# Optimization experiments

Measured on AMD Instinct MI355X. Metric: run time of the kernel, lower is better.

The kernel has to match this reference:

```python
import jax, jax.numpy as jnp
import numpy as np

MARGIN = 1.0


def setup_inputs() -> dict:
    key = jax.random.key(0)
    k1, k2, k3 = jax.random.split(key, 3)
    B, P = 8192, 16
    return {
        "energies": jax.random.normal(k1, (B, 1), dtype=jnp.float32),
        "property_values": jax.random.normal(k2, (B, P), dtype=jnp.float32),
        "property_targets": jax.random.normal(k3, (P,), dtype=jnp.float32),
    }


def reference(energies, property_values, property_targets):
    # distances[i] = ||property_values[i] - property_targets||_2, shape [B]
    distances = jnp.linalg.norm(property_values - property_targets[None, :], axis=-1)
    B = energies.shape[0]
    e = energies[:, 0]  # [B]
    # pair mask: i != j and distances[i] < distances[j]  -> [B, B]
    mask = (distances[:, None] < distances[None, :]) & (~jnp.eye(B, dtype=bool))
    # ranking loss per pair: relu(e_i - e_j + margin)
    pair_loss = jax.nn.relu(e[:, None] - e[None, :] + MARGIN)
    loss_sum = jnp.sum(jnp.where(mask, pair_loss, 0.0))
    count = jnp.sum(mask).astype(jnp.float32)
    loss = loss_sum / jnp.maximum(count, 1.0)
    # torch version accumulates [1]-shaped tensors -> output shape [1]
    return loss[None]
```

## Files before the change

### kernel.cpp

```cpp
#include <hip/hip_runtime.h>
#include <math.h>

#define MARGIN 1.0f
#define NT 256
#define TI 512
#define TJ 256

__global__ __launch_bounds__(NT) void dist_kernel(
    const float* __restrict__ pv,
    const float* __restrict__ pt,
    float* __restrict__ dist,
    float* __restrict__ acc,
    unsigned* __restrict__ counter,
    int B, int P)
{
    if (blockIdx.x == 0 && threadIdx.x == 0) {
        acc[0] = 0.f;
        *counter = 0u;
    }
    int i = blockIdx.x * NT + threadIdx.x;
    if (i >= B) return;
    float s = 0.f;
    if ((P & 3) == 0) {
        const float4* row = (const float4*)(pv + (size_t)i * P);
        const float4* tgt = (const float4*)pt;
        for (int p = 0; p < (P >> 2); ++p) {
            float4 v = row[p];
            float4 t = tgt[p];
            float d0 = v.x - t.x, d1 = v.y - t.y, d2 = v.z - t.z, d3 = v.w - t.w;
            s = fmaf(d0, d0, s); s = fmaf(d1, d1, s);
            s = fmaf(d2, d2, s); s = fmaf(d3, d3, s);
        }
    } else {
        const float* row = pv + (size_t)i * P;
        for (int p = 0; p < P; ++p) {
            float d = row[p] - pt[p];
            s = fmaf(d, d, s);
        }
    }
    dist[i] = sqrtf(s);
}

__global__ __launch_bounds__(NT) void pair_kernel(
    const float* __restrict__ e,
    const float* __restrict__ dist,
    float* __restrict__ acc,
    unsigned* __restrict__ counter,
    float* __restrict__ out,
    int B, int nj)
{
    __shared__ float2 sde[TJ];

    int it = blockIdx.x / nj;
    int jt = blockIdx.x % nj;

    {
        int j = jt * TJ + (int)threadIdx.x;
        bool ok = (j < B);
        float dj = ok ? dist[j] : -INFINITY;
        float ej = ok ? e[j]    : 0.f;
        sde[threadIdx.x] = make_float2(dj, ej);
    }
    __syncthreads();

    int i0 = it * TI + (int)threadIdx.x;
    int i1 = i0 + NT;
    bool ok0 = (i0 < B), ok1 = (i1 < B);
    float d0 = ok0 ? dist[i0] : INFINITY;
    float a0 = ok0 ? (e[i0] + MARGIN) : 0.f;
    float d1 = ok1 ? dist[i1] : INFINITY;
    float a1 = ok1 ? (e[i1] + MARGIN) : 0.f;

    const float4* sde4 = (const float4*)sde;
    float sum = 0.f;
    #pragma unroll 8
    for (int k = 0; k < TJ / 2; ++k) {
        float4 q = sde4[k];
        float w;
        w = (d0 < q.x) ? a0 : -INFINITY;  sum += fmaxf(w - q.y, 0.f);
        w = (d1 < q.x) ? a1 : -INFINITY;  sum += fmaxf(w - q.y, 0.f);
        w = (d0 < q.z) ? a0 : -INFINITY;  sum += fmaxf(w - q.w, 0.f);
        w = (d1 < q.z) ? a1 : -INFINITY;  sum += fmaxf(w - q.w, 0.f);
    }

    for (int off = 32; off > 0; off >>= 1)
        sum += __shfl_down(sum, off, 64);
    __shared__ float ws_sum[NT / 64];
    int wave = threadIdx.x >> 6;
    int lane = threadIdx.x & 63;
    if (lane == 0) ws_sum[wave] = sum;
    __syncthreads();

    if (threadIdx.x == 0) {
        float bsum = 0.f;
        for (int w = 0; w < NT / 64; ++w) bsum += ws_sum[w];
        atomicAdd(&acc[0], bsum);
        __threadfence();
        unsigned prev = atomicAdd(counter, 1u);
        if (prev == gridDim.x - 1) {
            float s = atomicAdd(&acc[0], 0.f);
            double cnt = 0.5 * (double)B * ((double)B - 1.0);
            if (cnt < 1.0) cnt = 1.0;
            out[0] = (float)((double)s / cnt);
        }
    }
}

extern "C" void kernel_launch(void* const* d_in, const int* in_sizes, int n_in,
                              void* d_out, int out_size, void* d_ws, size_t ws_size,
                              hipStream_t stream)
{
    const float* energies = (const float*)d_in[0];
    const float* pv       = (const float*)d_in[1];
    const float* pt       = (const float*)d_in[2];
    int B = in_sizes[0];
    int P = in_sizes[2];

    float*    acc     = (float*)d_ws;
    unsigned* counter = (unsigned*)d_ws + 2;
    float*    dist    = (float*)d_ws + 4;

    int ni = (B + TI - 1) / TI;
    int nj = (B + TJ - 1) / TJ;

    dist_kernel<<<(B + NT - 1) / NT, NT, 0, stream>>>(pv, pt, dist, acc, counter, B, P);
    pair_kernel<<<ni * nj, NT, 0, stream>>>(energies, dist, acc, counter,
                                            (float*)d_out, B, nj);
}
```

Measured before the change: 79.08 us.

## Fuse distance and pair kernels into one cooperative kernel with grid-sync reduction

The separate distance kernel is removed. Each pair block now computes the squared distances it needs for its i and j rows directly from property_values. The global atomic accumulator and last-block counter are replaced by per-block partial sums, a cooperative grid sync, and a final reduction in block 0. This drops one kernel launch and the distance buffer round-trip. In exchange, the distance arithmetic is repeated across blocks and a grid-wide barrier is added, which requires all 512 blocks to be co-resident.

```diff
diff --git a/kernel.cpp b/kernel.cpp
--- a/kernel.cpp
+++ b/kernel.cpp
@@ -1,75 +1,64 @@
 #include <hip/hip_runtime.h>
+#include <hip/hip_cooperative_groups.h>
 #include <math.h>
+
+namespace cg = cooperative_groups;
 
 #define MARGIN 1.0f
 #define NT 256
 #define TI 512
 #define TJ 256
 
-__global__ __launch_bounds__(NT) void dist_kernel(
+__global__ __launch_bounds__(NT) void fused_kernel(
+    const float* __restrict__ e,
     const float* __restrict__ pv,
     const float* __restrict__ pt,
-    float* __restrict__ dist,
-    float* __restrict__ acc,
-    unsigned* __restrict__ counter,
-    int B, int P)
-{
-    if (blockIdx.x == 0 && threadIdx.x == 0) {
-        acc[0] = 0.f;
-        *counter = 0u;
-    }
-    int i = blockIdx.x * NT + threadIdx.x;
-    if (i >= B) return;
-    float s = 0.f;
-    if ((P & 3) == 0) {
-        const float4* row = (const float4*)(pv + (size_t)i * P);
-        const float4* tgt = (const float4*)pt;
-        for (int p = 0; p < (P >> 2); ++p) {
-            float4 v = row[p];
-            float4 t = tgt[p];
-            float d0 = v.x - t.x, d1 = v.y - t.y, d2 = v.z - t.z, d3 = v.w - t.w;
-            s = fmaf(d0, d0, s); s = fmaf(d1, d1, s);
-            s = fmaf(d2, d2, s); s = fmaf(d3, d3, s);
-        }
-    } else {
-        const float* row = pv + (size_t)i * P;
-        for (int p = 0; p < P; ++p) {
-            float d = row[p] - pt[p];
-            s = fmaf(d, d, s);
-        }
-    }
-    dist[i] = sqrtf(s);
-}
-
-__global__ __launch_bounds__(NT) void pair_kernel(
-    const float* __restrict__ e,
-    const float* __restrict__ dist,
-    float* __restrict__ acc,
-    unsigned* __restrict__ counter,
+    float* __restrict__ psum,
     float* __restrict__ out,
-    int B, int nj)
+    int B, int P, int nj)
 {
     __shared__ float2 sde[TJ];
 
-    int it = blockIdx.x / nj;
-    int jt = blockIdx.x % nj;
+    const int it = blockIdx.x / nj;
+    const int jt = blockIdx.x % nj;
+
+    auto dist2 = [&](int row) -> float {
+        float s = 0.f;
+        if ((P & 3) == 0) {
+            const float4* r = (const float4*)(pv + (size_t)row * P);
+            const float4* t = (const float4*)pt;
+            for (int p = 0; p < (P >> 2); ++p) {
+                float4 v = r[p], g = t[p];
+                float a = v.x - g.x, b = v.y - g.y, c = v.z - g.z, d = v.w - g.w;
+                s = fmaf(a, a, s); s = fmaf(b, b, s);
+                s = fmaf(c, c, s); s = fmaf(d, d, s);
+            }
+        } else {
+            const float* r = pv + (size_t)row * P;
+            for (int p = 0; p < P; ++p) {
+                float d = r[p] - pt[p];
+                s = fmaf(d, d, s);
+            }
+        }
+        return s;
+    };
 
     {
         int j = jt * TJ + (int)threadIdx.x;
-        bool ok = (j < B);
-        float dj = ok ? dist[j] : -INFINITY;
-        float ej = ok ? e[j]    : 0.f;
+        float dj = -INFINITY, ej = 0.f;
+        if (j < B) { dj = dist2(j); ej = e[j]; }
         sde[threadIdx.x] = make_float2(dj, ej);
     }
-    __syncthreads();
 
     int i0 = it * TI + (int)threadIdx.x;
     int i1 = i0 + NT;
     bool ok0 = (i0 < B), ok1 = (i1 < B);
-    float d0 = ok0 ? dist[i0] : INFINITY;
+    float d0 = ok0 ? dist2(i0) : INFINITY;
     float a0 = ok0 ? (e[i0] + MARGIN) : 0.f;
-    float d1 = ok1 ? dist[i1] : INFINITY;
+    float d1 = ok1 ? dist2(i1) : INFINITY;
     float a1 = ok1 ? (e[i1] + MARGIN) : 0.f;
+
+    __syncthreads();
 
     const float4* sde4 = (const float4*)sde;
     float sum = 0.f;
@@ -90,18 +79,29 @@
     int lane = threadIdx.x & 63;
     if (lane == 0) ws_sum[wave] = sum;
     __syncthreads();
-
     if (threadIdx.x == 0) {
         float bsum = 0.f;
         for (int w = 0; w < NT / 64; ++w) bsum += ws_sum[w];
-        atomicAdd(&acc[0], bsum);
-        __threadfence();
-        unsigned prev = atomicAdd(counter, 1u);
-        if (prev == gridDim.x - 1) {
-            float s = atomicAdd(&acc[0], 0.f);
+        psum[blockIdx.x] = bsum;
+    }
+
+    cg::this_grid().sync();
+
+    if (blockIdx.x == 0) {
+        int nblk = (int)gridDim.x;
+        float s = 0.f;
+        for (int k = threadIdx.x; k < nblk; k += NT) s += psum[k];
+        for (int off = 32; off > 0; off >>= 1)
+            s += __shfl_down(s, off, 64);
+        __shared__ float fs[NT / 64];
+        if (lane == 0) fs[wave] = s;
+        __syncthreads();
+        if (threadIdx.x == 0) {
+            float tot = 0.f;
+            for (int w = 0; w < NT / 64; ++w) tot += fs[w];
             double cnt = 0.5 * (double)B * ((double)B - 1.0);
             if (cnt < 1.0) cnt = 1.0;
-            out[0] = (float)((double)s / cnt);
+            out[0] = (float)((double)tot / cnt);
         }
     }
 }
@@ -116,14 +116,16 @@
     int B = in_sizes[0];
     int P = in_sizes[2];
 
-    float*    acc     = (float*)d_ws;
-    unsigned* counter = (unsigned*)d_ws + 2;
-    float*    dist    = (float*)d_ws + 4;
-
     int ni = (B + TI - 1) / TI;
     int nj = (B + TJ - 1) / TJ;
+    int nblk = ni * nj;
 
-    dist_kernel<<<(B + NT - 1) / NT, NT, 0, stream>>>(pv, pt, dist, acc, counter, B, P);
-    pair_kernel<<<ni * nj, NT, 0, stream>>>(energies, dist, acc, counter,
-                                            (float*)d_out, B, nj);
+    float* psum = (float*)d_ws;
+    float* out  = (float*)d_out;
+
+    void* args[] = { (void*)&energies, (void*)&pv, (void*)&pt,
+                     (void*)&psum, (void*)&out,
+                     (void*)&B, (void*)&P, (void*)&nj };
+    hipLaunchCooperativeKernel((void*)fused_kernel, dim3(nblk), dim3(NT),
+                               args, 0, stream);
 }
```

Result: slower. 115.2 us (+45.7%).
